# Optimization experiments

Measured on AMD Instinct MI355X. Metric: run time of the kernel, lower is better.

The kernel has to match this reference:

```python
import jax, jax.numpy as jnp
import numpy as np

B, L, H, N = 256, 50, 128, 100000
NEG_MASK = -1.0e9  # value used by torch masked_fill_ on attention scores


def setup_inputs() -> dict:
    key = jax.random.key(0)
    ks = jax.random.split(key, 12)
    s = 1.0 / np.sqrt(H)
    return {
        "all_memory": jax.random.normal(ks[0], (B, L, H), jnp.float32),
        "last_memory": jax.random.normal(ks[1], (B, H), jnp.float32),
        "seq_item": jax.random.randint(ks[2], (B, L), 0, N),
        "mask": jnp.zeros((B, L), dtype=bool),
        # parameters (eval mode: dropout is identity)
        "Ue_w": jax.random.normal(ks[3], (H, H), jnp.float32) * s,
        "Ue_b": jnp.zeros((H,), jnp.float32),
        "We_w": jax.random.normal(ks[4], (H, H), jnp.float32) * s,
        "We_b": jnp.zeros((H,), jnp.float32),
        "Ve_w": jax.random.normal(ks[5], (H, 1), jnp.float32) * s,
        "Ve_b": jnp.zeros((1,), jnp.float32),
        "Wexp": jax.random.normal(ks[6], (2 * H, N), jnp.float32) * (1.0 / np.sqrt(2 * H)),
    }


def reference(all_memory, last_memory, seq_item, mask,
              Ue_w, Ue_b, We_w, We_b, Ve_w, Ve_b, Wexp):
    # Additive (Bahdanau) attention over the sequence
    a = jnp.einsum('blh,hk->blk', all_memory, Ue_w) + Ue_b          # [B,L,H]
    q = last_memory @ We_w + We_b                                    # [B,H]
    scores = jnp.squeeze(jnp.tanh(a + q[:, None, :]) @ Ve_w, -1) + Ve_b  # [B,L]
    scores = jnp.where(mask, NEG_MASK, scores)
    attn = jax.nn.softmax(scores, axis=1)                            # [B,L]
    ctx = jnp.einsum('bl,blh->bh', attn, all_memory)                 # [B,H]
    feat = jnp.concatenate([ctx, last_memory], axis=1)               # [B,2H]
    logits = feat @ Wexp                                             # [B,N]
    # explore mask: count of each item in the history (positions with item>0),
    # equivalent to bmm((seq_item>0), one_hot(seq_item)) without the dense one-hot
    valid = (seq_item > 0).astype(logits.dtype)                      # [B,L]
    counts = jnp.zeros((B, N), logits.dtype).at[
        jnp.arange(B)[:, None], seq_item].add(valid)                 # [B,N]
    logits = jnp.where(counts > 0, -jnp.inf, logits)
    return jax.nn.softmax(logits, axis=1)
```

## Files before the change

kernel.cpp:

```cpp
#include <hip/hip_runtime.h>
#include <math.h>

#define B_ 256
#define L_ 50
#define H_ 128
#define N_ 100000
#define K_ 256
#define NREP 64

typedef __attribute__((ext_vector_type(8))) short short8;
typedef __attribute__((ext_vector_type(4))) float f32x4;

__device__ inline short f2bf(float x) {
  union { float f; unsigned u; } v; v.f = x;
  unsigned r = (v.u + 0x7fff + ((v.u >> 16) & 1)) >> 16;
  return (short)r;
}
__device__ inline float bf2f(short h) {
  union { unsigned u; float f; } v; v.u = ((unsigned)(unsigned short)h) << 16;
  return v.f;
}

#define GLD_ROW_TO_LDS(g, l) __builtin_amdgcn_global_load_lds(                 \
    (const __attribute__((address_space(1))) void*)(g),                        \
    (__attribute__((address_space(3))) void*)(l), 4, 0, 0)

__global__ __launch_bounds__(256)
void attn_feat_kernel(const float* __restrict__ am, const float* __restrict__ lm,
    const float* __restrict__ Ue_w, const float* __restrict__ Ue_b,
    const float* __restrict__ We_w, const float* __restrict__ We_b,
    const float* __restrict__ Ve_w, const float* __restrict__ Ve_b,
    const unsigned char* __restrict__ mask,
    short* __restrict__ feat_hi, short* __restrict__ feat_lo,
    float* __restrict__ sums_rep)
{
  const int b = blockIdx.x;
  const int t = threadIdx.x;
  __shared__ float UeS[H_ * H_];
  __shared__ float amS[L_][H_];
  __shared__ float lmS[H_], qS[H_];
  __shared__ float attnS[64];
  __shared__ float redW[4][32];

  if (t < 64) sums_rep[b * 64 + t] = 0.0f;

  for (int i = t; i < H_ * H_ / 4; i += 256)
    ((float4*)UeS)[i] = ((const float4*)Ue_w)[i];
  for (int i = t; i < L_ * H_ / 4; i += 256)
    ((float4*)amS)[i] = ((const float4*)(am + (size_t)b * L_ * H_))[i];
  if (t < H_) lmS[t] = lm[b * H_ + t];
  __syncthreads();

  if (t < H_) {
    float q = We_b[t];
    #pragma unroll 8
    for (int h = 0; h < H_; ++h) q += lmS[h] * We_w[h * H_ + t];
    qS[t] = q;
  }
  __syncthreads();

  const int k = t & 127, half = t >> 7, wv = t >> 6, lk = t & 63;
  const float ve  = Ve_w[k];
  const float ueb = Ue_b[k];
  const float veb = Ve_b[0];
  for (int li = 0; li < 25; ++li) {
    const int l = half * 25 + li;
    float a = ueb;
    #pragma unroll 8
    for (int h = 0; h < H_; ++h) a = fmaf(amS[l][h], UeS[h * H_ + k], a);
    float v = tanhf(a + qS[k]) * ve;
    #pragma unroll
    for (int off = 32; off > 0; off >>= 1) v += __shfl_down(v, off, 64);
    if (lk == 0) redW[wv][li] = v;
  }
  __syncthreads();
  if (t < 50) {
    const int hf = t / 25, li = t - hf * 25;
    attnS[t] = redW[hf * 2][li] + redW[hf * 2 + 1][li] + veb;
  }
  __syncthreads();

  if (t < 64) {
    float s = (t < L_) ? attnS[t] : -3.0e38f;
    if (t < L_ && mask[b * L_ + t]) s = -1.0e9f;
    float m = s;
    #pragma unroll
    for (int off = 32; off > 0; off >>= 1) m = fmaxf(m, __shfl_xor(m, off));
    float e = (t < L_) ? __expf(s - m) : 0.0f;
    float tot = e;
    #pragma unroll
    for (int off = 32; off > 0; off >>= 1) tot += __shfl_xor(tot, off);
    if (t < L_) attnS[t] = e / tot;
  }
  __syncthreads();

  if (t < H_) {
    float c = 0.0f;
    #pragma unroll
    for (int l = 0; l < L_; ++l) c = fmaf(attnS[l], amS[l][t], c);
    short h1 = f2bf(c);
    feat_hi[b * K_ + t] = h1;
    feat_lo[b * K_ + t] = f2bf(c - bf2f(h1));
    float lv = lmS[t];
    short h2 = f2bf(lv);
    feat_hi[b * K_ + H_ + t] = h2;
    feat_lo[b * K_ + H_ + t] = f2bf(lv - bf2f(h2));
  }
}

#define TN 64
#define TNP 66
#define KC 64

__global__ __launch_bounds__(256)
void logits_mfma_kernel(const short* __restrict__ feat_hi, const short* __restrict__ feat_lo,
                        const float* __restrict__ Wexp, float* __restrict__ out,
                        float* __restrict__ sums_rep)
{
  __shared__ float wbuf[2][KC * TNP];
  const int t = threadIdx.x;
  const int lane = t & 63, w = t >> 6;
  const int ln = t & 15, quad = (t >> 4) & 3;
  const int n0 = blockIdx.x * TN;
  const bool tail = (n0 + TN > N_);

  f32x4 acc[4][4];
  #pragma unroll
  for (int i = 0; i < 4; ++i)
    #pragma unroll
    for (int j = 0; j < 4; ++j) acc[i][j] = (f32x4)(0.0f);

  #define STAGE(bufi, kc)                                                      \
    do {                                                                       \
      if (!tail) {                                                             \
        const float* g0 = Wexp + (size_t)((kc) + w * 16) * N_ + n0 + lane;     \
        float* l0 = &wbuf[bufi][(w * 16) * TNP];                               \
        _Pragma("unroll")                                                      \
        for (int i = 0; i < 16; ++i)                                           \
          GLD_ROW_TO_LDS(g0 + (size_t)i * N_, l0 + i * TNP);                   \
      } else {                                                                 \
        for (int i = t; i < KC * TN; i += 256) {                               \
          int kk_ = i >> 6, nn_ = i & 63;                                      \
          int gn = n0 + nn_;                                                   \
          wbuf[bufi][kk_ * TNP + nn_] =                                        \
              (gn < N_) ? Wexp[(size_t)((kc) + kk_) * N_ + gn] : 0.0f;         \
        }                                                                      \
      }                                                                        \
    } while (0)

  STAGE(0, 0);

  #pragma unroll
  for (int c = 0; c < K_ / KC; ++c) {
    __syncthreads();
    if (c + 1 < K_ / KC) STAGE((c + 1) & 1, (c + 1) * KC);
    const int cb = c & 1;
    const int kc = c * KC;

    #pragma unroll
    for (int kk = 0; kk < KC; kk += 32) {
      short8 ah[4], al[4];
      const int kof = kc + kk + quad * 8;
      #pragma unroll
      for (int mt = 0; mt < 4; ++mt) {
        const int m = w * 64 + mt * 16 + ln;
        ah[mt] = *(const short8*)(feat_hi + m * K_ + kof);
        al[mt] = *(const short8*)(feat_lo + m * K_ + kof);
      }
      short8 bh[4], bl[4];
      #pragma unroll
      for (int nt = 0; nt < 4; ++nt) {
        #pragma unroll
        for (int j = 0; j < 8; ++j) {
          const float v = wbuf[cb][(kk + quad * 8 + j) * TNP + nt * 16 + ln];
          const short h = f2bf(v);
          bh[nt][j] = h;
          bl[nt][j] = f2bf(v - bf2f(h));
        }
      }
      #pragma unroll
      for (int mt = 0; mt < 4; ++mt)
        #pragma unroll
        for (int nt = 0; nt < 4; ++nt) {
          acc[mt][nt] = __builtin_amdgcn_mfma_f32_16x16x32_bf16(ah[mt], bh[nt], acc[mt][nt], 0, 0, 0);
          acc[mt][nt] = __builtin_amdgcn_mfma_f32_16x16x32_bf16(ah[mt], bl[nt], acc[mt][nt], 0, 0, 0);
          acc[mt][nt] = __builtin_amdgcn_mfma_f32_16x16x32_bf16(al[mt], bh[nt], acc[mt][nt], 0, 0, 0);
        }
    }
  }

  float rs[4][4];
  #pragma unroll
  for (int mt = 0; mt < 4; ++mt)
    #pragma unroll
    for (int r = 0; r < 4; ++r) rs[mt][r] = 0.0f;

  #pragma unroll
  for (int mt = 0; mt < 4; ++mt) {
    #pragma unroll
    for (int nt = 0; nt < 4; ++nt) {
      const int col = n0 + nt * 16 + ln;
      #pragma unroll
      for (int r = 0; r < 4; ++r) {
        const int row = w * 64 + mt * 16 + quad * 4 + r;
        const float e = __expf(acc[mt][nt][r]);
        if (col < N_) {
          out[(size_t)row * N_ + col] = e;
          rs[mt][r] += e;
        }
      }
    }
  }
  #pragma unroll
  for (int off = 8; off > 0; off >>= 1)
    #pragma unroll
    for (int mt = 0; mt < 4; ++mt)
      #pragma unroll
      for (int r = 0; r < 4; ++r) rs[mt][r] += __shfl_down(rs[mt][r], off, 16);
  if (ln == 0) {
    float* rep = sums_rep + (blockIdx.x & (NREP - 1)) * 256;
    #pragma unroll
    for (int mt = 0; mt < 4; ++mt)
      #pragma unroll
      for (int r = 0; r < 4; ++r)
        atomicAdd(&rep[w * 64 + mt * 16 + quad * 4 + r], rs[mt][r]);
  }
}

__global__ __launch_bounds__(256)
void reduce_sums_kernel(const float* __restrict__ sums_rep, float* __restrict__ sums)
{
  const int b = threadIdx.x;
  float s = 0.0f;
  #pragma unroll
  for (int r = 0; r < NREP; ++r) s += sums_rep[r * 256 + b];
  sums[b] = s;
}

__global__ __launch_bounds__(256)
void mask_kernel(const int* __restrict__ seq, float* __restrict__ out, float* __restrict__ sums)
{
  int idx = blockIdx.x * 256 + threadIdx.x;
  if (idx >= B_ * L_) return;
  int b = idx / L_;
  int item = seq[idx];
  if (item > 0) {
    float old = atomicExch(&out[(size_t)b * N_ + item], 0.0f);
    if (old != 0.0f) atomicAdd(&sums[b], -old);
  }
}

#define NV4 (N_ / 4)
__global__ __launch_bounds__(256)
void norm_kernel(float* __restrict__ out, const float* __restrict__ sums)
{
  const int b = blockIdx.y;
  const float inv = 1.0f / sums[b];
  float4* row = (float4*)(out + (size_t)b * N_);
  const int i0 = blockIdx.x * (256 * 4) + threadIdx.x;
  #pragma unroll
  for (int u = 0; u < 4; ++u) {
    const int i = i0 + u * 256;
    if (i < NV4) {
      float4 v = row[i];
      v.x *= inv; v.y *= inv; v.z *= inv; v.w *= inv;
      row[i] = v;
    }
  }
}

extern "C" void kernel_launch(void* const* d_in, const int* in_sizes, int n_in,
                              void* d_out, int out_size, void* d_ws, size_t ws_size,
                              hipStream_t stream)
{
  const float* am   = (const float*)d_in[0];
  const float* lm   = (const float*)d_in[1];
  const int*   seq  = (const int*)d_in[2];
  const unsigned char* mask = (const unsigned char*)d_in[3];
  const float* Ue_w = (const float*)d_in[4];
  const float* Ue_b = (const float*)d_in[5];
  const float* We_w = (const float*)d_in[6];
  const float* We_b = (const float*)d_in[7];
  const float* Ve_w = (const float*)d_in[8];
  const float* Ve_b = (const float*)d_in[9];
  const float* Wexp = (const float*)d_in[10];
  float* out = (float*)d_out;

  short* feat_hi  = (short*)d_ws;
  short* feat_lo  = feat_hi + B_ * K_;
  float* sums_rep = (float*)(feat_lo + B_ * K_);
  float* sums     = sums_rep + NREP * 256;

  attn_feat_kernel<<<B_, 256, 0, stream>>>(am, lm, Ue_w, Ue_b, We_w, We_b,
                                           Ve_w, Ve_b, mask, feat_hi, feat_lo, sums_rep);
  logits_mfma_kernel<<<(N_ + TN - 1) / TN, 256, 0, stream>>>(feat_hi, feat_lo, Wexp, out, sums_rep);
  reduce_sums_kernel<<<1, 256, 0, stream>>>(sums_rep, sums);
  mask_kernel<<<(B_ * L_ + 255) / 256, 256, 0, stream>>>(seq, out, sums);
  dim3 gN((NV4 + 256 * 4 - 1) / (256 * 4), B_);
  norm_kernel<<<gN, 256, 0, stream>>>(out, sums);
}
```

Baseline: 395.1 us.

## Register-stage Wexp, convert once to bf16 hi/lo in swizzled LDS

```diff
diff --git a/kernel.cpp b/kernel.cpp
--- a/kernel.cpp
+++ b/kernel.cpp
@@ -20,10 +20,6 @@
   union { unsigned u; float f; } v; v.u = ((unsigned)(unsigned short)h) << 16;
   return v.f;
 }
-
-#define GLD_ROW_TO_LDS(g, l) __builtin_amdgcn_global_load_lds(                 \
-    (const __attribute__((address_space(1))) void*)(g),                        \
-    (__attribute__((address_space(3))) void*)(l), 4, 0, 0)
 
 __global__ __launch_bounds__(256)
 void attn_feat_kernel(const float* __restrict__ am, const float* __restrict__ lm,
@@ -109,7 +105,6 @@
 }
 
 #define TN 64
-#define TNP 66
 #define KC 64
 
 __global__ __launch_bounds__(256)
@@ -117,43 +112,72 @@
                         const float* __restrict__ Wexp, float* __restrict__ out,
                         float* __restrict__ sums_rep)
 {
-  __shared__ float wbuf[2][KC * TNP];
+  __shared__ __align__(16) short bhS[2][TN * KC];
+  __shared__ __align__(16) short blS[2][TN * KC];
+
   const int t = threadIdx.x;
-  const int lane = t & 63, w = t >> 6;
+  const int w = t >> 6;
   const int ln = t & 15, quad = (t >> 4) & 3;
   const int n0 = blockIdx.x * TN;
   const bool tail = (n0 + TN > N_);
 
+  const int sn  = t & 63;
+  const int skb = (t >> 6) << 4;
+  const int ssx = (sn & 7) << 4;
+
   f32x4 acc[4][4];
   #pragma unroll
   for (int i = 0; i < 4; ++i)
     #pragma unroll
     for (int j = 0; j < 4; ++j) acc[i][j] = (f32x4)(0.0f);
 
-  #define STAGE(bufi, kc)                                                      \
+  float r[16];
+
+  #define LOADC(kc_)                                                           \
     do {                                                                       \
       if (!tail) {                                                             \
-        const float* g0 = Wexp + (size_t)((kc) + w * 16) * N_ + n0 + lane;     \
-        float* l0 = &wbuf[bufi][(w * 16) * TNP];                               \
+        const float* g = Wexp + (size_t)((kc_) + skb) * N_ + n0 + sn;          \
         _Pragma("unroll")                                                      \
-        for (int i = 0; i < 16; ++i)                                           \
-          GLD_ROW_TO_LDS(g0 + (size_t)i * N_, l0 + i * TNP);                   \
+        for (int i = 0; i < 16; ++i) r[i] = g[(size_t)i * N_];                 \
       } else {                                                                 \
-        for (int i = t; i < KC * TN; i += 256) {                               \
-          int kk_ = i >> 6, nn_ = i & 63;                                      \
-          int gn = n0 + nn_;                                                   \
-          wbuf[bufi][kk_ * TNP + nn_] =                                        \
-              (gn < N_) ? Wexp[(size_t)((kc) + kk_) * N_ + gn] : 0.0f;         \
+        const bool ok = (n0 + sn) < N_;                                        \
+        const int gn = ok ? (n0 + sn) : (N_ - 1);          \
+        const float* g = Wexp + (size_t)((kc_) + skb) * N_ + gn;               \
+        _Pragma("unroll")                                                      \
+        for (int i = 0; i < 16; ++i) { float v = g[(size_t)i * N_]; r[i] = ok ? v : 0.0f; } \
+      }                                                                        \
+    } while (0)
+
+  #define CONVW(bufi)                                                          \
+    do {                                                                       \
+      short8 h2[2], l2[2];                                                     \
+      _Pragma("unroll")                                                        \
+      for (int c_ = 0; c_ < 2; ++c_) {                                         \
+        _Pragma("unroll")                                                      \
+        for (int j_ = 0; j_ < 8; ++j_) {                                       \
+          union { float f; unsigned u; } v_; v_.f = r[c_ * 8 + j_];            \
+          union { unsigned u; float f; } hv_; hv_.u = v_.u & 0xffff0000u;      \
+          h2[c_][j_] = (short)(v_.u >> 16);                                    \
+          l2[c_][j_] = f2bf(v_.f - hv_.f);                                     \
         }                                                                      \
       }                                                                        \
+      char* ph_ = (char*)&bhS[bufi][0] + sn * 128;                             \
+      char* pl_ = (char*)&blS[bufi][0] + sn * 128;                             \
+      *(short8*)(ph_ + ((skb * 2)      ^ ssx)) = h2[0];                        \
+      *(short8*)(ph_ + ((skb * 2 + 16) ^ ssx)) = h2[1];                        \
+      *(short8*)(pl_ + ((skb * 2)      ^ ssx)) = l2[0];                        \
+      *(short8*)(pl_ + ((skb * 2 + 16) ^ ssx)) = l2[1];                        \
     } while (0)
 
-  STAGE(0, 0);
+  #define LGKM_BARRIER() asm volatile("s_waitcnt lgkmcnt(0)\n\ts_barrier" ::: "memory")
+
+  LOADC(0);
+  CONVW(0);
+  LOADC(KC);
+  LGKM_BARRIER();
 
   #pragma unroll
   for (int c = 0; c < K_ / KC; ++c) {
-    __syncthreads();
-    if (c + 1 < K_ / KC) STAGE((c + 1) & 1, (c + 1) * KC);
     const int cb = c & 1;
     const int kc = c * KC;
 
@@ -170,13 +194,10 @@
       short8 bh[4], bl[4];
       #pragma unroll
       for (int nt = 0; nt < 4; ++nt) {
-        #pragma unroll
-        for (int j = 0; j < 8; ++j) {
-          const float v = wbuf[cb][(kk + quad * 8 + j) * TNP + nt * 16 + ln];
-          const short h = f2bf(v);
-          bh[nt][j] = h;
-          bl[nt][j] = f2bf(v - bf2f(h));
-        }
+        const int n = nt * 16 + ln;
+        const int off = (kk * 2 + quad * 16) ^ ((n & 7) << 4);
+        bh[nt] = *(const short8*)((const char*)&bhS[cb][0] + n * 128 + off);
+        bl[nt] = *(const short8*)((const char*)&blS[cb][0] + n * 128 + off);
       }
       #pragma unroll
       for (int mt = 0; mt < 4; ++mt)
@@ -187,13 +208,19 @@
           acc[mt][nt] = __builtin_amdgcn_mfma_f32_16x16x32_bf16(al[mt], bh[nt], acc[mt][nt], 0, 0, 0);
         }
     }
+
+    if (c + 1 < K_ / KC) {
+      CONVW((c + 1) & 1);
+      if (c + 2 < K_ / KC) LOADC((c + 2) * KC);
+      LGKM_BARRIER();
+    }
   }
 
   float rs[4][4];
   #pragma unroll
   for (int mt = 0; mt < 4; ++mt)
     #pragma unroll
-    for (int r = 0; r < 4; ++r) rs[mt][r] = 0.0f;
+    for (int r_ = 0; r_ < 4; ++r_) rs[mt][r_] = 0.0f;
 
   #pragma unroll
   for (int mt = 0; mt < 4; ++mt) {
@@ -201,12 +228,12 @@
     for (int nt = 0; nt < 4; ++nt) {
       const int col = n0 + nt * 16 + ln;
       #pragma unroll
-      for (int r = 0; r < 4; ++r) {
-        const int row = w * 64 + mt * 16 + quad * 4 + r;
-        const float e = __expf(acc[mt][nt][r]);
+      for (int r_ = 0; r_ < 4; ++r_) {
+        const int row = w * 64 + mt * 16 + quad * 4 + r_;
+        const float e = __expf(acc[mt][nt][r_]);
         if (col < N_) {
           out[(size_t)row * N_ + col] = e;
-          rs[mt][r] += e;
+          rs[mt][r_] += e;
         }
       }
     }
@@ -216,14 +243,14 @@
     #pragma unroll
     for (int mt = 0; mt < 4; ++mt)
       #pragma unroll
-      for (int r = 0; r < 4; ++r) rs[mt][r] += __shfl_down(rs[mt][r], off, 16);
+      for (int r_ = 0; r_ < 4; ++r_) rs[mt][r_] += __shfl_down(rs[mt][r_], off, 16);
   if (ln == 0) {
     float* rep = sums_rep + (blockIdx.x & (NREP - 1)) * 256;
     #pragma unroll
     for (int mt = 0; mt < 4; ++mt)
       #pragma unroll
-      for (int r = 0; r < 4; ++r)
-        atomicAdd(&rep[w * 64 + mt * 16 + quad * 4 + r], rs[mt][r]);
+      for (int r_ = 0; r_ < 4; ++r_)
+        atomicAdd(&rep[w * 64 + mt * 16 + quad * 4 + r_], rs[mt][r_]);
   }
 }
 
```

After: 368.9 us. 6.6% less time.

## Swap MFMA operand roles, load Wexp directly to registers, vectorize output stores

Applied to the files above, without the earlier changes.

```diff
diff --git a/kernel.cpp b/kernel.cpp
--- a/kernel.cpp
+++ b/kernel.cpp
@@ -20,10 +20,6 @@
   union { unsigned u; float f; } v; v.u = ((unsigned)(unsigned short)h) << 16;
   return v.f;
 }
-
-#define GLD_ROW_TO_LDS(g, l) __builtin_amdgcn_global_load_lds(                 \
-    (const __attribute__((address_space(1))) void*)(g),                        \
-    (__attribute__((address_space(3))) void*)(l), 4, 0, 0)
 
 __global__ __launch_bounds__(256)
 void attn_feat_kernel(const float* __restrict__ am, const float* __restrict__ lm,
@@ -109,122 +105,117 @@
 }
 
 #define TN 64
-#define TNP 66
-#define KC 64
 
 __global__ __launch_bounds__(256)
 void logits_mfma_kernel(const short* __restrict__ feat_hi, const short* __restrict__ feat_lo,
                         const float* __restrict__ Wexp, float* __restrict__ out,
                         float* __restrict__ sums_rep)
 {
-  __shared__ float wbuf[2][KC * TNP];
   const int t = threadIdx.x;
-  const int lane = t & 63, w = t >> 6;
-  const int ln = t & 15, quad = (t >> 4) & 3;
+  const int w = t >> 6;
+  const int lane = t & 63;
+  const int ln = lane & 15, quad = lane >> 4;
   const int n0 = blockIdx.x * TN;
   const bool tail = (n0 + TN > N_);
 
+  int coff[4];
+  float msk[4];
+  #pragma unroll
+  for (int mt = 0; mt < 4; ++mt) {
+    int c = n0 + mt * 16 + ln;
+    msk[mt] = (c < N_) ? 1.0f : 0.0f;
+    coff[mt] = (c < N_) ? c : (N_ - 1);
+  }
+
+  const short* fh0 = feat_hi + ((size_t)(w * 64 + ln)) * K_ + quad * 8;
+  const short* fl0 = feat_lo + ((size_t)(w * 64 + ln)) * K_ + quad * 8;
+
   f32x4 acc[4][4];
   #pragma unroll
   for (int i = 0; i < 4; ++i)
     #pragma unroll
     for (int j = 0; j < 4; ++j) acc[i][j] = (f32x4)(0.0f);
 
-  #define STAGE(bufi, kc)                                                      \
+  float wreg[2][32];
+
+  #define LOADW(bi, s_)                                                        \
     do {                                                                       \
-      if (!tail) {                                                             \
-        const float* g0 = Wexp + (size_t)((kc) + w * 16) * N_ + n0 + lane;     \
-        float* l0 = &wbuf[bufi][(w * 16) * TNP];                               \
+      const float* gp = Wexp + (size_t)((s_) * 32 + quad * 8) * N_;            \
+      _Pragma("unroll")                                                        \
+      for (int mt = 0; mt < 4; ++mt)                                           \
         _Pragma("unroll")                                                      \
-        for (int i = 0; i < 16; ++i)                                           \
-          GLD_ROW_TO_LDS(g0 + (size_t)i * N_, l0 + i * TNP);                   \
-      } else {                                                                 \
-        for (int i = t; i < KC * TN; i += 256) {                               \
-          int kk_ = i >> 6, nn_ = i & 63;                                      \
-          int gn = n0 + nn_;                                                   \
-          wbuf[bufi][kk_ * TNP + nn_] =                                        \
-              (gn < N_) ? Wexp[(size_t)((kc) + kk_) * N_ + gn] : 0.0f;         \
+        for (int j = 0; j < 8; ++j)                                            \
+          wreg[bi][mt * 8 + j] = gp[(size_t)j * N_ + coff[mt]];                \
+    } while (0)
+
+  #define STEP(s_, bi)                                                         \
+    do {                                                                       \
+      short8 fbh[4], fbl[4];                                                   \
+      _Pragma("unroll")                                                        \
+      for (int nt = 0; nt < 4; ++nt) {                                         \
+        fbh[nt] = *(const short8*)(fh0 + (size_t)nt * 16 * K_ + (s_) * 32);    \
+        fbl[nt] = *(const short8*)(fl0 + (size_t)nt * 16 * K_ + (s_) * 32);    \
+      }                                                                        \
+      short8 wa_h[4], wa_l[4];                                                 \
+      _Pragma("unroll")                                                        \
+      for (int mt = 0; mt < 4; ++mt) {                                         \
+        _Pragma("unroll")                                                      \
+        for (int j = 0; j < 8; ++j) {                                          \
+          float f = wreg[bi][mt * 8 + j];                                      \
+          if (tail) f *= msk[mt];                                              \
+          union { float f; unsigned u; } v_; v_.f = f;                         \
+          union { unsigned u; float f; } h_; h_.u = v_.u & 0xffff0000u;        \
+          wa_h[mt][j] = (short)(v_.u >> 16);                                   \
+          wa_l[mt][j] = f2bf(f - h_.f);                                        \
         }                                                                      \
       }                                                                        \
+      _Pragma("unroll")                                                        \
+      for (int mt = 0; mt < 4; ++mt)                                           \
+        _Pragma("unroll")                                                      \
+        for (int nt = 0; nt < 4; ++nt) {                                       \
+          acc[mt][nt] = __builtin_amdgcn_mfma_f32_16x16x32_bf16(wa_h[mt], fbh[nt], acc[mt][nt], 0, 0, 0); \
+          acc[mt][nt] = __builtin_amdgcn_mfma_f32_16x16x32_bf16(wa_l[mt], fbh[nt], acc[mt][nt], 0, 0, 0); \
+          acc[mt][nt] = __builtin_amdgcn_mfma_f32_16x16x32_bf16(wa_h[mt], fbl[nt], acc[mt][nt], 0, 0, 0); \
+        }                                                                      \
     } while (0)
 
-  STAGE(0, 0);
-
-  #pragma unroll
-  for (int c = 0; c < K_ / KC; ++c) {
-    __syncthreads();
-    if (c + 1 < K_ / KC) STAGE((c + 1) & 1, (c + 1) * KC);
-    const int cb = c & 1;
-    const int kc = c * KC;
-
-    #pragma unroll
-    for (int kk = 0; kk < KC; kk += 32) {
-      short8 ah[4], al[4];
-      const int kof = kc + kk + quad * 8;
-      #pragma unroll
-      for (int mt = 0; mt < 4; ++mt) {
-        const int m = w * 64 + mt * 16 + ln;
-        ah[mt] = *(const short8*)(feat_hi + m * K_ + kof);
-        al[mt] = *(const short8*)(feat_lo + m * K_ + kof);
+  LOADW(0, 0);
+  #pragma unroll
+  for (int s = 0; s < 8; ++s) {
+    if (s < 7) LOADW((s + 1) & 1, s + 1);
+    STEP(s, s & 1);
+  }
+
+  float rs[4] = {0.0f, 0.0f, 0.0f, 0.0f};
+  #pragma unroll
+  for (int mt = 0; mt < 4; ++mt) {
+    const int c0 = n0 + mt * 16 + quad * 4;
+    const bool ok = c0 < N_;
+    #pragma unroll
+    for (int nt = 0; nt < 4; ++nt) {
+      float4 ev;
+      float s4;
+      {
+        const float e0 = __expf(acc[mt][nt][0]);
+        const float e1 = __expf(acc[mt][nt][1]);
+        const float e2 = __expf(acc[mt][nt][2]);
+        const float e3 = __expf(acc[mt][nt][3]);
+        ev.x = e0; ev.y = e1; ev.z = e2; ev.w = e3;
+        s4 = (e0 + e1) + (e2 + e3);
       }
-      short8 bh[4], bl[4];
-      #pragma unroll
-      for (int nt = 0; nt < 4; ++nt) {
-        #pragma unroll
-        for (int j = 0; j < 8; ++j) {
-          const float v = wbuf[cb][(kk + quad * 8 + j) * TNP + nt * 16 + ln];
-          const short h = f2bf(v);
-          bh[nt][j] = h;
-          bl[nt][j] = f2bf(v - bf2f(h));
-        }
-      }
-      #pragma unroll
-      for (int mt = 0; mt < 4; ++mt)
-        #pragma unroll
-        for (int nt = 0; nt < 4; ++nt) {
-          acc[mt][nt] = __builtin_amdgcn_mfma_f32_16x16x32_bf16(ah[mt], bh[nt], acc[mt][nt], 0, 0, 0);
-          acc[mt][nt] = __builtin_amdgcn_mfma_f32_16x16x32_bf16(ah[mt], bl[nt], acc[mt][nt], 0, 0, 0);
-          acc[mt][nt] = __builtin_amdgcn_mfma_f32_16x16x32_bf16(al[mt], bh[nt], acc[mt][nt], 0, 0, 0);
-        }
-    }
-  }
-
-  float rs[4][4];
-  #pragma unroll
-  for (int mt = 0; mt < 4; ++mt)
-    #pragma unroll
-    for (int r = 0; r < 4; ++r) rs[mt][r] = 0.0f;
-
-  #pragma unroll
-  for (int mt = 0; mt < 4; ++mt) {
-    #pragma unroll
-    for (int nt = 0; nt < 4; ++nt) {
-      const int col = n0 + nt * 16 + ln;
-      #pragma unroll
-      for (int r = 0; r < 4; ++r) {
-        const int row = w * 64 + mt * 16 + quad * 4 + r;
-        const float e = __expf(acc[mt][nt][r]);
-        if (col < N_) {
-          out[(size_t)row * N_ + col] = e;
-          rs[mt][r] += e;
-        }
+      if (ok) {
+        *(float4*)(out + (size_t)(w * 64 + nt * 16 + ln) * N_ + c0) = ev;
+        rs[nt] += s4;
       }
     }
   }
   #pragma unroll
-  for (int off = 8; off > 0; off >>= 1)
-    #pragma unroll
-    for (int mt = 0; mt < 4; ++mt)
-      #pragma unroll
-      for (int r = 0; r < 4; ++r) rs[mt][r] += __shfl_down(rs[mt][r], off, 16);
-  if (ln == 0) {
-    float* rep = sums_rep + (blockIdx.x & (NREP - 1)) * 256;
-    #pragma unroll
-    for (int mt = 0; mt < 4; ++mt)
-      #pragma unroll
-      for (int r = 0; r < 4; ++r)
-        atomicAdd(&rep[w * 64 + mt * 16 + quad * 4 + r], rs[mt][r]);
-  }
+  for (int nt = 0; nt < 4; ++nt) {
+    rs[nt] += __shfl_xor(rs[nt], 16, 64);
+    rs[nt] += __shfl_xor(rs[nt], 32, 64);
+  }
+  const float mine = (quad == 0) ? rs[0] : (quad == 1) ? rs[1] : (quad == 2) ? rs[2] : rs[3];
+  atomicAdd(&sums_rep[(size_t)(blockIdx.x & (NREP - 1)) * 256 + w * 64 + lane], mine);
 }
 
 __global__ __launch_bounds__(256)
```

Result: no change. 393.5 us (-0.4%).

## Retile logits GEMM: feat in swizzled LDS, Wexp streamed to registers

Applied to the files above, without the earlier changes.

```diff
diff --git a/kernel.cpp b/kernel.cpp
--- a/kernel.cpp
+++ b/kernel.cpp
@@ -20,10 +20,6 @@
   union { unsigned u; float f; } v; v.u = ((unsigned)(unsigned short)h) << 16;
   return v.f;
 }
-
-#define GLD_ROW_TO_LDS(g, l) __builtin_amdgcn_global_load_lds(                 \
-    (const __attribute__((address_space(1))) void*)(g),                        \
-    (__attribute__((address_space(3))) void*)(l), 4, 0, 0)
 
 __global__ __launch_bounds__(256)
 void attn_feat_kernel(const float* __restrict__ am, const float* __restrict__ lm,
@@ -108,21 +104,62 @@
   }
 }
 
-#define TN 64
-#define TNP 66
-#define KC 64
-
-__global__ __launch_bounds__(256)
+#define TNW 64
+#define WAVES 8
+#define TNB (TNW * WAVES)
+#define MBR 64
+#define NBX ((N_ + TNB - 1) / TNB)
+
+__global__ __launch_bounds__(512, 2)
 void logits_mfma_kernel(const short* __restrict__ feat_hi, const short* __restrict__ feat_lo,
                         const float* __restrict__ Wexp, float* __restrict__ out,
                         float* __restrict__ sums_rep)
 {
-  __shared__ float wbuf[2][KC * TNP];
+  __shared__ __align__(16) short fhS[MBR * K_];
+  __shared__ __align__(16) short flS[MBR * K_];
+
   const int t = threadIdx.x;
-  const int lane = t & 63, w = t >> 6;
-  const int ln = t & 15, quad = (t >> 4) & 3;
-  const int n0 = blockIdx.x * TN;
-  const bool tail = (n0 + TN > N_);
+  const int w = t >> 6, lane = t & 63, ln = lane & 15, quad = lane >> 4;
+  const int m0 = blockIdx.y * MBR;
+  const int n0w = blockIdx.x * TNB + w * TNW;
+  const bool tail = (n0w + TNW > N_);
+
+  int coff[4]; float cmask[4];
+  #pragma unroll
+  for (int nt = 0; nt < 4; ++nt) {
+    const int c = n0w + nt * 16 + ln;
+    cmask[nt] = (c < N_) ? 1.0f : 0.0f;
+    coff[nt] = (c < N_) ? c : (N_ - 1);
+  }
+
+  float wreg[2][32];
+
+  #define LOADW(bi, s_)                                                        \
+    do {                                                                       \
+      const float* gp = Wexp + (size_t)((s_) * 32 + quad * 8) * N_;            \
+      _Pragma("unroll")                                                        \
+      for (int nt = 0; nt < 4; ++nt)                                           \
+        _Pragma("unroll")                                                      \
+        for (int j = 0; j < 8; ++j)                                            \
+          wreg[bi][nt * 8 + j] = gp[(size_t)j * N_ + coff[nt]];                \
+    } while (0)
+
+  LOADW(0, 0);
+
+  {
+    const int slot = t & 31;
+    const int row0 = t >> 5;
+    #pragma unroll
+    for (int i = 0; i < 4; ++i) {
+      const int row = row0 + i * 16;
+      const short8 vh = *(const short8*)(feat_hi + (size_t)(m0 + row) * K_ + slot * 8);
+      const short8 vl = *(const short8*)(feat_lo + (size_t)(m0 + row) * K_ + slot * 8);
+      const int byte = (row * 512 + slot * 16) ^ ((row & 7) << 4);
+      *(short8*)((char*)fhS + byte) = vh;
+      *(short8*)((char*)flS + byte) = vl;
+    }
+  }
+  __syncthreads();
 
   f32x4 acc[4][4];
   #pragma unroll
@@ -130,85 +167,63 @@
     #pragma unroll
     for (int j = 0; j < 4; ++j) acc[i][j] = (f32x4)(0.0f);
 
-  #define STAGE(bufi, kc)                                                      \
-    do {                                                                       \
-      if (!tail) {                                                             \
-        const float* g0 = Wexp + (size_t)((kc) + w * 16) * N_ + n0 + lane;     \
-        float* l0 = &wbuf[bufi][(w * 16) * TNP];                               \
-        _Pragma("unroll")                                                      \
-        for (int i = 0; i < 16; ++i)                                           \
-          GLD_ROW_TO_LDS(g0 + (size_t)i * N_, l0 + i * TNP);                   \
-      } else {                                                                 \
-        for (int i = t; i < KC * TN; i += 256) {                               \
-          int kk_ = i >> 6, nn_ = i & 63;                                      \
-          int gn = n0 + nn_;                                                   \
-          wbuf[bufi][kk_ * TNP + nn_] =                                        \
-              (gn < N_) ? Wexp[(size_t)((kc) + kk_) * N_ + gn] : 0.0f;         \
-        }                                                                      \
-      }                                                                        \
-    } while (0)
-
-  STAGE(0, 0);
-
-  #pragma unroll
-  for (int c = 0; c < K_ / KC; ++c) {
-    __syncthreads();
-    if (c + 1 < K_ / KC) STAGE((c + 1) & 1, (c + 1) * KC);
-    const int cb = c & 1;
-    const int kc = c * KC;
-
-    #pragma unroll
-    for (int kk = 0; kk < KC; kk += 32) {
-      short8 ah[4], al[4];
-      const int kof = kc + kk + quad * 8;
+  #pragma unroll
+  for (int s = 0; s < 8; ++s) {
+    if (s < 7) LOADW((s + 1) & 1, s + 1);
+    const int bi = s & 1;
+
+    short8 bh[4], bl[4];
+    #pragma unroll
+    for (int nt = 0; nt < 4; ++nt) {
       #pragma unroll
-      for (int mt = 0; mt < 4; ++mt) {
-        const int m = w * 64 + mt * 16 + ln;
-        ah[mt] = *(const short8*)(feat_hi + m * K_ + kof);
-        al[mt] = *(const short8*)(feat_lo + m * K_ + kof);
+      for (int j = 0; j < 8; ++j) {
+        float f = wreg[bi][nt * 8 + j];
+        if (tail) f *= cmask[nt];
+        union { float f; unsigned u; } v_; v_.f = f;
+        union { unsigned u; float f; } h_; h_.u = v_.u & 0xffff0000u;
+        bh[nt][j] = (short)(v_.u >> 16);
+        bl[nt][j] = f2bf(f - h_.f);
       }
-      short8 bh[4], bl[4];
+    }
+
+    short8 ah[4], al[4];
+    #pragma unroll
+    for (int mt = 0; mt < 4; ++mt) {
+      const int byte = ((mt * 16 + ln) * 512 + s * 64 + quad * 16) ^ ((ln & 7) << 4);
+      ah[mt] = *(const short8*)((const char*)fhS + byte);
+      al[mt] = *(const short8*)((const char*)flS + byte);
+    }
+
+    #pragma unroll
+    for (int mt = 0; mt < 4; ++mt)
       #pragma unroll
       for (int nt = 0; nt < 4; ++nt) {
-        #pragma unroll
-        for (int j = 0; j < 8; ++j) {
-          const float v = wbuf[cb][(kk + quad * 8 + j) * TNP + nt * 16 + ln];
-          const short h = f2bf(v);
-          bh[nt][j] = h;
-          bl[nt][j] = f2bf(v - bf2f(h));
+        acc[mt][nt] = __builtin_amdgcn_mfma_f32_16x16x32_bf16(ah[mt], bh[nt], acc[mt][nt], 0, 0, 0);
+        acc[mt][nt] = __builtin_amdgcn_mfma_f32_16x16x32_bf16(ah[mt], bl[nt], acc[mt][nt], 0, 0, 0);
+        acc[mt][nt] = __builtin_amdgcn_mfma_f32_16x16x32_bf16(al[mt], bh[nt], acc[mt][nt], 0, 0, 0);
+      }
+  }
+
+  float rs[4][4];
+  #pragma unroll
+  for (int mt = 0; mt < 4; ++mt)
+    #pragma unroll
+    for (int r_ = 0; r_ < 4; ++r_) rs[mt][r_] = 0.0f;
+
+  #pragma unroll
+  for (int mt = 0; mt < 4; ++mt) {
+    #pragma unroll
+    for (int nt = 0; nt < 4; ++nt) {
+      const int col = n0w + nt * 16 + ln;
+      #pragma unroll
+      for (int r_ = 0; r_ < 4; ++r_) {
+        const int row = m0 + mt * 16 + quad * 4 + r_;
+        const float e = __expf(acc[mt][nt][r_]);
+        if (col < N_) {
+          out[(size_t)row * N_ + col] = e;
+          rs[mt][r_] += e;
         }
       }
-      #pragma unroll
-      for (int mt = 0; mt < 4; ++mt)
-        #pragma unroll
-        for (int nt = 0; nt < 4; ++nt) {
-          acc[mt][nt] = __builtin_amdgcn_mfma_f32_16x16x32_bf16(ah[mt], bh[nt], acc[mt][nt], 0, 0, 0);
-          acc[mt][nt] = __builtin_amdgcn_mfma_f32_16x16x32_bf16(ah[mt], bl[nt], acc[mt][nt], 0, 0, 0);
-          acc[mt][nt] = __builtin_amdgcn_mfma_f32_16x16x32_bf16(al[mt], bh[nt], acc[mt][nt], 0, 0, 0);
-        }
-    }
-  }
-
-  float rs[4][4];
-  #pragma unroll
-  for (int mt = 0; mt < 4; ++mt)
-    #pragma unroll
-    for (int r = 0; r < 4; ++r) rs[mt][r] = 0.0f;
-
-  #pragma unroll
-  for (int mt = 0; mt < 4; ++mt) {
-    #pragma unroll
-    for (int nt = 0; nt < 4; ++nt) {
-      const int col = n0 + nt * 16 + ln;
-      #pragma unroll
-      for (int r = 0; r < 4; ++r) {
-        const int row = w * 64 + mt * 16 + quad * 4 + r;
-        const float e = __expf(acc[mt][nt][r]);
-        if (col < N_) {
-          out[(size_t)row * N_ + col] = e;
-          rs[mt][r] += e;
-        }
-      }
     }
   }
   #pragma unroll
@@ -216,15 +231,16 @@
     #pragma unroll
     for (int mt = 0; mt < 4; ++mt)
       #pragma unroll
-      for (int r = 0; r < 4; ++r) rs[mt][r] += __shfl_down(rs[mt][r], off, 16);
-  if (ln == 0) {
-    float* rep = sums_rep + (blockIdx.x & (NREP - 1)) * 256;
-    #pragma unroll
-    for (int mt = 0; mt < 4; ++mt)
-      #pragma unroll
-      for (int r = 0; r < 4; ++r)
-        atomicAdd(&rep[w * 64 + mt * 16 + quad * 4 + r], rs[mt][r]);
-  }
+      for (int r_ = 0; r_ < 4; ++r_) rs[mt][r_] += __shfl_xor(rs[mt][r_], off, 64);
+
+  const int my_mt = ln >> 2, my_r = ln & 3;
+  const float v0_ = (my_r == 0) ? rs[0][0] : (my_r == 1) ? rs[0][1] : (my_r == 2) ? rs[0][2] : rs[0][3];
+  const float v1_ = (my_r == 0) ? rs[1][0] : (my_r == 1) ? rs[1][1] : (my_r == 2) ? rs[1][2] : rs[1][3];
+  const float v2_ = (my_r == 0) ? rs[2][0] : (my_r == 1) ? rs[2][1] : (my_r == 2) ? rs[2][2] : rs[2][3];
+  const float v3_ = (my_r == 0) ? rs[3][0] : (my_r == 1) ? rs[3][1] : (my_r == 2) ? rs[3][2] : rs[3][3];
+  const float myv = (my_mt == 0) ? v0_ : (my_mt == 1) ? v1_ : (my_mt == 2) ? v2_ : v3_;
+  const int myrow = m0 + my_mt * 16 + quad * 4 + my_r;
+  atomicAdd(&sums_rep[(size_t)(blockIdx.x & (NREP - 1)) * 256 + myrow], myv);
 }
 
 __global__ __launch_bounds__(256)
@@ -293,7 +309,8 @@
 
   attn_feat_kernel<<<B_, 256, 0, stream>>>(am, lm, Ue_w, Ue_b, We_w, We_b,
                                            Ve_w, Ve_b, mask, feat_hi, feat_lo, sums_rep);
-  logits_mfma_kernel<<<(N_ + TN - 1) / TN, 256, 0, stream>>>(feat_hi, feat_lo, Wexp, out, sums_rep);
+  dim3 gB(NBX, B_ / MBR);
+  logits_mfma_kernel<<<gB, 512, 0, stream>>>(feat_hi, feat_lo, Wexp, out, sums_rep);
   reduce_sums_kernel<<<1, 256, 0, stream>>>(sums_rep, sums);
   mask_kernel<<<(B_ * L_ + 255) / 256, 256, 0, stream>>>(seq, out, sums);
   dim3 gN((NV4 + 256 * 4 - 1) / (256 * 4), B_);
```

After: 365.8 us. 1.08x faster.
